# Kernel optimization log

Hardware: AMD Instinct MI355X
Metric: run time of the kernel (lower is better)

Reference implementation:

```python
import jax, jax.numpy as jnp
import numpy as np

N, E, H, IN_NF, G, STEPS, EHID = 4096, 8192, 128, 64, 8, 3, 32


def setup_inputs() -> dict:
    key = jax.random.key(0)
    ks = jax.random.split(key, 24)

    def gn(k, shape, fan_in):
        return jax.random.normal(k, shape, dtype=jnp.float32) / np.sqrt(fan_in)

    inp = {
        "x": jax.random.normal(ks[0], (N, IN_NF), dtype=jnp.float32),
        "edge_index": jax.random.randint(ks[1], (2, E), 0, N, dtype=jnp.int32),
        "edge_attr": jax.random.uniform(ks[2], (E, 1), dtype=jnp.float32),
        "batch": jnp.sort(jax.random.randint(ks[3], (N,), 0, G, dtype=jnp.int32)),
        # lin0: in_nf -> hid
        "lin0_w": gn(ks[4], (IN_NF, H), IN_NF),
        "lin0_b": jnp.zeros((H,), jnp.float32),
        # per-step edge MLP: 1 -> 32 -> H*H (stacked over STEPS)
        "nn_w1": gn(ks[5], (STEPS, 1, EHID), 1),
        "nn_b1": jnp.zeros((STEPS, EHID), jnp.float32),
        "nn_w2": gn(ks[6], (STEPS, EHID, H * H), EHID) * 0.1,
        "nn_b2": jnp.zeros((STEPS, H * H), jnp.float32),
        # NNConv root weight (no bias) + conv bias, per step
        "root_w": gn(ks[7], (STEPS, H, H), H),
        "conv_b": jnp.zeros((STEPS, H), jnp.float32),
        # single-layer GRU (input H, hidden H); gate order r, z, n
        "gru_wih": gn(ks[8], (3 * H, H), H),
        "gru_whh": gn(ks[9], (3 * H, H), H),
        "gru_bih": jnp.zeros((3 * H,), jnp.float32),
        "gru_bhh": jnp.zeros((3 * H,), jnp.float32),
        # readout
        "lin1_w": gn(ks[10], (H, H // 2), H),
        "lin1_b": jnp.zeros((H // 2,), jnp.float32),
        "lin2_w": gn(ks[11], (H // 2, 1), H // 2),
        "lin2_b": jnp.zeros((1,), jnp.float32),
    }
    return inp


def _gru_cell(m, h, wih, whh, bih, bhh):
    gi = m @ wih.T + bih          # [N, 3H]
    gh = h @ whh.T + bhh          # [N, 3H]
    i_r, i_z, i_n = jnp.split(gi, 3, axis=-1)
    h_r, h_z, h_n = jnp.split(gh, 3, axis=-1)
    r = jax.nn.sigmoid(i_r + h_r)
    z = jax.nn.sigmoid(i_z + h_z)
    n = jnp.tanh(i_n + r * h_n)
    return (1.0 - z) * n + z * h


def reference(x, edge_index, edge_attr, batch, lin0_w, lin0_b, nn_w1, nn_b1,
              nn_w2, nn_b2, root_w, conv_b, gru_wih, gru_whh, gru_bih,
              gru_bhh, lin1_w, lin1_b, lin2_w, lin2_b):
    n_nodes = x.shape[0]
    row, col = edge_index[0], edge_index[1]  # source j -> target i

    x = jax.nn.relu(x @ lin0_w + lin0_b)     # [N, H]
    h = x

    # in-degree for mean aggregation (0-degree nodes -> 0 output)
    deg = jax.ops.segment_sum(jnp.ones((row.shape[0],), x.dtype), col,
                              num_segments=n_nodes)
    inv_deg = jnp.where(deg > 0, 1.0 / jnp.maximum(deg, 1.0), 0.0)[:, None]

    for t in range(STEPS):
        # edge-conditioned weights: [E, H, H]
        e_h = jax.nn.relu(edge_attr @ nn_w1[t] + nn_b1[t])
        w_e = (e_h @ nn_w2[t] + nn_b2[t]).reshape(-1, H, H)
        # gather -> per-edge matvec -> scatter-mean
        msg = jnp.einsum('eh,eho->eo', x[row], w_e)
        agg = jax.ops.segment_sum(msg, col, num_segments=n_nodes) * inv_deg
        m = jax.nn.relu(agg + x @ root_w[t] + conv_b[t])
        h = _gru_cell(m, h, gru_wih, gru_whh, gru_bih, gru_bhh)
        x = h

    # global mean pool over graphs
    cnt = jax.ops.segment_sum(jnp.ones((n_nodes,), x.dtype), batch,
                              num_segments=G)
    g = jax.ops.segment_sum(x, batch, num_segments=G) / jnp.maximum(cnt, 1.0)[:, None]
    g = jax.nn.relu(g @ lin1_w + lin1_b)  # dropout: eval mode (identity)
    out = g @ lin2_w + lin2_b             # [G, 1]
    return out
```

## Files before the change

### kernel.cpp

```cpp
#include <hip/hip_runtime.h>
#include <math.h>

#define NN 4096
#define EE 8192
#define HH 128
#define GG 8
#define MU 4096

typedef __attribute__((ext_vector_type(8))) _Float16 half8;
typedef __attribute__((ext_vector_type(4))) float floatx4;

__device__ __forceinline__ void ldst16(const _Float16* g, void* l) {
    __builtin_amdgcn_global_load_lds(
        (const __attribute__((address_space(1))) unsigned int*)g,
        (__attribute__((address_space(3))) unsigned int*)l, 16, 0, 0);
}

__device__ __forceinline__ int cls_k(float w, float b, float mn, float mx) {
    const float hi = w > 0.f ? w * mx + b : w * mn + b;
    const float lo = w > 0.f ? w * mn + b : w * mx + b;
    if (hi <= 0.f) return 0;
    if (lo >= 0.f) return 1;
    return 2;
}

__device__ __forceinline__ void ea_range(const float* eattr, float* sred,
                                         float& mn, float& mx) {
    const int t = threadIdx.x;
    float mxl = -1e30f, mnl = 1e30f;
    for (int i = t; i < EE; i += 256) {
        const float v = eattr[i];
        mxl = fmaxf(mxl, v); mnl = fminf(mnl, v);
    }
    sred[t] = mxl; __syncthreads();
    for (int d = 128; d > 0; d >>= 1) {
        if (t < d) sred[t] = fmaxf(sred[t], sred[t + d]);
        __syncthreads();
    }
    mx = sred[0]; __syncthreads();
    sred[t] = mnl; __syncthreads();
    for (int d = 128; d > 0; d >>= 1) {
        if (t < d) sred[t] = fminf(sred[t], sred[t + d]);
        __syncthreads();
    }
    mn = sred[0]; __syncthreads();
}

__global__ __launch_bounds__(256) void ymix_gh_k(
    const _Float16* __restrict__ A, const _Float16* __restrict__ BT3t,
    const _Float16* __restrict__ Bhh, const float* __restrict__ bhh,
    const float* __restrict__ w2t, _Float16* __restrict__ Y,
    float* __restrict__ g2, _Float16* __restrict__ U,
    float* __restrict__ mpre, const int* __restrict__ kflag)
{
    __shared__ __align__(16) _Float16 As[128 * 32];
    __shared__ __align__(16) _Float16 Bs[128 * 32];
    const int tid = threadIdx.x;
    const int lane = tid & 63, wave = tid >> 6;
    const int m0 = blockIdx.y * 128;
    const int wr = (wave >> 1) * 64, wc = (wave & 1) * 64;
    const int fm = lane & 15, fq = lane >> 4;
    const int srow = tid >> 2, soff = (tid & 3) << 3;
    const _Float16* gA0 = A + (size_t)(m0 + srow) * 128 + soff;
    const _Float16* gA1 = gA0 + (size_t)64 * 128;
    char* lA0 = (char*)As + tid * 16;  char* lA1 = (char*)As + (tid + 256) * 16;
    char* lB0 = (char*)Bs + tid * 16;  char* lB1 = (char*)Bs + (tid + 256) * 16;
    const int bx = blockIdx.x;
    const int er = fq * 4, ec = fm;

    const int bid = blockIdx.y * gridDim.x + blockIdx.x;
    const int nbl = gridDim.x * gridDim.y;
    for (int i = bid * 256 + tid; i < 131072; i += nbl * 256)
        ((float4*)mpre)[i] = make_float4(0.f, 0.f, 0.f, 0.f);

    floatx4 acc[4][4] = {};
    if (bx < 6) {
        const _Float16* gB0 = (bx < 3)
            ? BT3t + (size_t)(bx * 128 + srow) * 128 + soff
            : Bhh + (size_t)((bx - 3) * 128 + srow) * 128 + soff;
        const _Float16* gB1 = gB0 + (size_t)64 * 128;
        for (int k0 = 0; k0 < 128; k0 += 32) {
            __syncthreads();
            ldst16(gA0 + k0, lA0); ldst16(gA1 + k0, lA1);
            ldst16(gB0 + k0, lB0); ldst16(gB1 + k0, lB1);
            __syncthreads();
            half8 af[4], bf[4];
#pragma unroll
            for (int i = 0; i < 4; ++i)
                af[i] = *(const half8*)&As[(wr + i * 16 + fm) * 32 + fq * 8];
#pragma unroll
            for (int j = 0; j < 4; ++j)
                bf[j] = *(const half8*)&Bs[(wc + j * 16 + fm) * 32 + fq * 8];
#pragma unroll
            for (int i = 0; i < 4; ++i)
#pragma unroll
                for (int j = 0; j < 4; ++j)
                    acc[i][j] = __builtin_amdgcn_mfma_f32_16x16x32_f16(
                        af[i], bf[j], acc[i][j], 0, 0, 0);
        }
        if (bx < 3) {
#pragma unroll
            for (int i = 0; i < 4; ++i) {
                const int gr = m0 + wr + i * 16 + er;
#pragma unroll
                for (int j = 0; j < 4; ++j) {
                    const int gc = bx * 128 + wc + j * 16 + ec;
#pragma unroll
                    for (int r = 0; r < 4; ++r)
                        Y[(size_t)(gr + r) * 384 + gc] = (_Float16)acc[i][j][r];
                }
            }
        } else {
            const int n0 = (bx - 3) * 128;
#pragma unroll
            for (int i = 0; i < 4; ++i) {
                const int gr = m0 + wr + i * 16 + er;
#pragma unroll
                for (int j = 0; j < 4; ++j) {
                    const int gc = n0 + wc + j * 16 + ec;
                    const float bv = bhh[gc];
#pragma unroll
                    for (int r = 0; r < 4; ++r)
                        g2[(size_t)(gr + r) * 384 + gc] = acc[i][j][r] + bv;
                }
            }
        }
    } else {
        const unsigned f = *(const unsigned*)kflag;
        const int kk = bx - 6;
        if (!((f >> kk) & 1u)) return;
        const int cbase = __popc(f & ((1u << kk) - 1u)) << 7;
        const float* w2s = w2t + (size_t)kk * 16384;
        for (int k0 = 0; k0 < 128; k0 += 32) {
            __syncthreads();
            ldst16(gA0 + k0, lA0); ldst16(gA1 + k0, lA1);
#pragma unroll
            for (int c = tid; c < 512; c += 256) {
                const int row = c >> 2, seg = (c & 3) << 3;
                _Float16 v8[8];
#pragma unroll
                for (int u = 0; u < 8; ++u)
                    v8[u] = (_Float16)w2s[(size_t)(k0 + seg + u) * 128 + row];
                *(half8*)&Bs[row * 32 + seg] = *(half8*)v8;
            }
            __syncthreads();
            half8 af[4], bf[4];
#pragma unroll
            for (int i = 0; i < 4; ++i)
                af[i] = *(const half8*)&As[(wr + i * 16 + fm) * 32 + fq * 8];
#pragma unroll
            for (int j = 0; j < 4; ++j)
                bf[j] = *(const half8*)&Bs[(wc + j * 16 + fm) * 32 + fq * 8];
#pragma unroll
            for (int i = 0; i < 4; ++i)
#pragma unroll
                for (int j = 0; j < 4; ++j)
                    acc[i][j] = __builtin_amdgcn_mfma_f32_16x16x32_f16(
                        af[i], bf[j], acc[i][j], 0, 0, 0);
        }
#pragma unroll
        for (int i = 0; i < 4; ++i) {
            const int gr = m0 + wr + i * 16 + er;
#pragma unroll
            for (int j = 0; j < 4; ++j) {
                const int gc = cbase + wc + j * 16 + ec;
#pragma unroll
                for (int r = 0; r < 4; ++r)
                    U[(size_t)(gr + r) * MU + gc] = (_Float16)acc[i][j][r];
            }
        }
    }
}

__global__ __launch_bounds__(256) void escat_k(
    const int* __restrict__ ei, const float* __restrict__ eattr,
    const float* __restrict__ deg, const float* __restrict__ ehPt,
    const _Float16* __restrict__ Y, const _Float16* __restrict__ U,
    float* __restrict__ mpre, const int* __restrict__ kflag)
{
    const int e = blockIdx.x * 2 + (threadIdx.x >> 7);
    const int o = threadIdx.x & 127;
    const int src = ei[e], dst = ei[EE + e];
    const float dv = deg[dst];
    const float inv = dv > 0.f ? 1.0f / dv : 0.0f;
    const float ea = eattr[e];
    const _Float16* Yr = Y + (size_t)src * 384;
    float acc = ea * inv * (float)Yr[o] + inv * (float)Yr[128 + o];
    const unsigned f = *(const unsigned*)kflag;
    if (f) {
        const int nk = __popc(f);
        const _Float16* Ur = U + (size_t)src * MU;
        const float* ep = ehPt + (size_t)e * 32;
        for (int i = 0; i < nk; ++i)
            acc += ep[i] * (float)Ur[i * 128 + o];
    }
    atomicAdd(&mpre[(size_t)dst * 128 + o], acc);
}

__global__ __launch_bounds__(256) void gruz0_k(
    const float* __restrict__ mpre, const _Float16* __restrict__ Y,
    const float* __restrict__ cb, const _Float16* __restrict__ Bih,
    const float* __restrict__ bih, float* __restrict__ g1)
{
    __shared__ __align__(16) _Float16 As[128 * 40];
    __shared__ __align__(16) _Float16 Bs[128 * 40];
    const int tid = threadIdx.x;
    const int lane = tid & 63, wave = tid >> 6;
    const int m0 = blockIdx.y * 128, n0 = blockIdx.x * 128;
    const int wr = (wave >> 1) * 64, wc = (wave & 1) * 64;
    const int fm = lane & 15, fq = lane >> 4;

    floatx4 acc[4][4] = {};
    for (int k0 = 0; k0 < 128; k0 += 32) {
        __syncthreads();
#pragma unroll
        for (int c = tid; c < 512; c += 256) {
            const int row = c >> 2, seg = (c & 3) << 3;
            const int mr = m0 + row;
            const half8 yv = *(const half8*)&Y[(size_t)mr * 384 + 256 + k0 + seg];
            const float4 a0 = *(const float4*)&mpre[(size_t)mr * 128 + k0 + seg];
            const float4 a1 = *(const float4*)&mpre[(size_t)mr * 128 + k0 + seg + 4];
            const float4 c0 = *(const float4*)&cb[k0 + seg];
            const float4 c1 = *(const float4*)&cb[k0 + seg + 4];
            _Float16 v8[8];
            float v;
            v = (float)yv[0] + a0.x + c0.x; v8[0] = (_Float16)(v > 0.f ? v : 0.f);
            v = (float)yv[1] + a0.y + c0.y; v8[1] = (_Float16)(v > 0.f ? v : 0.f);
            v = (float)yv[2] + a0.z + c0.z; v8[2] = (_Float16)(v > 0.f ? v : 0.f);
            v = (float)yv[3] + a0.w + c0.w; v8[3] = (_Float16)(v > 0.f ? v : 0.f);
            v = (float)yv[4] + a1.x + c1.x; v8[4] = (_Float16)(v > 0.f ? v : 0.f);
            v = (float)yv[5] + a1.y + c1.y; v8[5] = (_Float16)(v > 0.f ? v : 0.f);
            v = (float)yv[6] + a1.z + c1.z; v8[6] = (_Float16)(v > 0.f ? v : 0.f);
            v = (float)yv[7] + a1.w + c1.w; v8[7] = (_Float16)(v > 0.f ? v : 0.f);
            *(half8*)&As[row * 40 + seg] = *(half8*)v8;
            *(half8*)&Bs[row * 40 + seg] =
                *(const half8*)&Bih[(size_t)(n0 + row) * 128 + k0 + seg];
        }
        __syncthreads();
        half8 af[4], bf[4];
#pragma unroll
        for (int i = 0; i < 4; ++i)
            af[i] = *(const half8*)&As[(wr + i * 16 + fm) * 40 + fq * 8];
#pragma unroll
        for (int j = 0; j < 4; ++j)
            bf[j] = *(const half8*)&Bs[(wc + j * 16 + fm) * 40 + fq * 8];
#pragma unroll
        for (int i = 0; i < 4; ++i)
#pragma unroll
            for (int j = 0; j < 4; ++j)
                acc[i][j] = __builtin_amdgcn_mfma_f32_16x16x32_f16(
                    af[i], bf[j], acc[i][j], 0, 0, 0);
    }
    const int er = fq * 4, ec = fm;
#pragma unroll
    for (int i = 0; i < 4; ++i) {
        const int gr = m0 + wr + i * 16 + er;
#pragma unroll
        for (int j = 0; j < 4; ++j) {
            const int gc = n0 + wc + j * 16 + ec;
            const float bv = bih[gc];
#pragma unroll
            for (int r = 0; r < 4; ++r)
                g1[(size_t)(gr + r) * 384 + gc] = acc[i][j][r] + bv;
        }
    }
}

__global__ void gate_k(const float* __restrict__ G1, const float* __restrict__ G2,
                       float* __restrict__ xh, _Float16* __restrict__ Ax,
                       const int* __restrict__ batch, float* __restrict__ pooled) {
    const int idx = blockIdx.x * 256 + threadIdx.x;
    const int n = idx >> 7, o = idx & 127;
    const size_t b = (size_t)n * 384;
    float ir = G1[b + o], iz = G1[b + 128 + o], in_ = G1[b + 256 + o];
    float hr = G2[b + o], hz = G2[b + 128 + o], hn = G2[b + 256 + o];
    float r = 1.f / (1.f + expf(-(ir + hr)));
    float z = 1.f / (1.f + expf(-(iz + hz)));
    float nv = tanhf(in_ + r * hn);
    float hv = (1.f - z) * nv + z * xh[idx];
    xh[idx] = hv;
    Ax[idx] = (_Float16)hv;
    if (pooled) atomicAdd(&pooled[batch[n] * 128 + o], hv);
}

__global__ __launch_bounds__(256) void setup_all_k(
    const float* __restrict__ wih, const float* __restrict__ whh,
    _Float16* __restrict__ Bih, _Float16* __restrict__ Bhh,
    const int* __restrict__ ei, const float* __restrict__ eattr,
    const int* __restrict__ batch, float* __restrict__ deg,
    float* __restrict__ cnt,
    const float* __restrict__ x, const float* __restrict__ l0w,
    const float* __restrict__ l0b, float* __restrict__ xh,
    _Float16* __restrict__ Ax,
    const float* __restrict__ w1, const float* __restrict__ b1,
    const float* __restrict__ w2, const float* __restrict__ b2,
    const float* __restrict__ rw, _Float16* __restrict__ BT3,
    float* __restrict__ ehP, int* __restrict__ kflag)
{
    __shared__ float loc8[GG];
    __shared__ float As[16][64];
    __shared__ float Bs[16][64];
    __shared__ float sred[256];
    __shared__ float wl[32], bl[32];
    __shared__ unsigned mm[3];
    const int b = blockIdx.x, t = threadIdx.x;
    if (b < 192) {
        const int idx = b * 256 + t;
        Bih[idx] = (_Float16)wih[idx];
        Bhh[idx] = (_Float16)whh[idx];
    } else if (b < 224) {
        const int e = (b - 192) * 256 + t;
        atomicAdd(&deg[ei[EE + e]], 1.0f);
    } else if (b < 240) {
        const int n = (b - 224) * 256 + t;
        if (t < GG) loc8[t] = 0.f;
        __syncthreads();
        atomicAdd(&loc8[batch[n]], 1.0f);
        __syncthreads();
        if (t < GG) atomicAdd(&cnt[t], loc8[t]);
    } else if (b < 368) {
        const int bb = b - 240;
        const int j0 = (bb & 1) * 64;
        const int m0 = (bb >> 1) * 64;
        const int tx = t & 15, ty = t >> 4;
        const int arow = t >> 2, acol = (t & 3) << 2;
        const int bk = t >> 4, bj = (t & 15) << 2;
        float c[4][4] = {};
        for (int k0 = 0; k0 < 64; k0 += 16) {
            __syncthreads();
            float4 av = *(const float4*)&x[(size_t)(m0 + arow) * 64 + k0 + acol];
            As[acol + 0][arow] = av.x;
            As[acol + 1][arow] = av.y;
            As[acol + 2][arow] = av.z;
            As[acol + 3][arow] = av.w;
            *(float4*)&Bs[bk][bj] = *(const float4*)&l0w[(size_t)(k0 + bk) * 128 + j0 + bj];
            __syncthreads();
#pragma unroll
            for (int kk = 0; kk < 16; ++kk) {
                const float4 a = *(const float4*)&As[kk][ty << 2];
                const float4 bv = *(const float4*)&Bs[kk][tx << 2];
                c[0][0] += a.x * bv.x; c[0][1] += a.x * bv.y; c[0][2] += a.x * bv.z; c[0][3] += a.x * bv.w;
                c[1][0] += a.y * bv.x; c[1][1] += a.y * bv.y; c[1][2] += a.y * bv.z; c[1][3] += a.y * bv.w;
                c[2][0] += a.z * bv.x; c[2][1] += a.z * bv.y; c[2][2] += a.z * bv.z; c[2][3] += a.z * bv.w;
                c[3][0] += a.w * bv.x; c[3][1] += a.w * bv.y; c[3][2] += a.w * bv.z; c[3][3] += a.w * bv.w;
            }
        }
        const float4 bv = *(const float4*)&l0b[j0 + (tx << 2)];
        const int col0 = j0 + (tx << 2);
#pragma unroll
        for (int i = 0; i < 4; ++i) {
            const int row = m0 + (ty << 2) + i;
            float4 o;
            o.x = fmaxf(c[i][0] + bv.x, 0.f); o.y = fmaxf(c[i][1] + bv.y, 0.f);
            o.z = fmaxf(c[i][2] + bv.z, 0.f); o.w = fmaxf(c[i][3] + bv.w, 0.f);
            *(float4*)&xh[(size_t)row * 128 + col0] = o;
            _Float16* base = Ax + (size_t)row * 128 + col0;
            base[0] = (_Float16)o.x; base[1] = (_Float16)o.y;
            base[2] = (_Float16)o.z; base[3] = (_Float16)o.w;
        }
    } else if (b < 560) {
        float mn, mx;
        ea_range(eattr, sred, mn, mx);
        const int bb = b - 368;
        const int st = bb >> 6;
        if (t < 32) {
            const float w = w1[st * 32 + t], bv = b1[st * 32 + t];
            const int c = cls_k(w, bv, mn, mx);
            wl[t] = (c == 1) ? w : 0.f;
            bl[t] = (c == 1) ? bv : 0.f;
        }
        __syncthreads();
        const int idx = (bb & 63) * 256 + t;
        const int h = idx >> 7, o = idx & 127;
        const float* W2t = w2 + (size_t)st * 524288;
        float a = 0.f, c2 = 0.f;
#pragma unroll 8
        for (int j = 0; j < 32; ++j) {
            const float v = W2t[(size_t)j * 16384 + idx];
            a += wl[j] * v; c2 += bl[j] * v;
        }
        c2 += b2[(size_t)st * 16384 + idx];
        _Float16* B = BT3 + (size_t)st * 49152;
        B[(size_t)o * 128 + h]         = (_Float16)a;
        B[(size_t)(128 + o) * 128 + h] = (_Float16)c2;
        B[(size_t)(256 + o) * 128 + h] = (_Float16)rw[(size_t)st * 16384 + idx];
    } else if (b == 560) {
        float mn, mx;
        ea_range(eattr, sred, mn, mx);
        if (t < 3) mm[t] = 0u;
        __syncthreads();
        if (t < 96) {
            const int tt = t >> 5, k = t & 31;
            if (cls_k(w1[tt * 32 + k], b1[tt * 32 + k], mn, mx) == 2)
                atomicOr(&mm[tt], 1u << k);
        }
        __syncthreads();
        if (t < 3) kflag[t] = (int)mm[t];
    } else {
        float mn, mx;
        ea_range(eattr, sred, mn, mx);
        if (t < 3) mm[t] = 0u;
        __syncthreads();
        if (t < 96) {
            const int tt = t >> 5, k = t & 31;
            if (cls_k(w1[tt * 32 + k], b1[tt * 32 + k], mn, mx) == 2)
                atomicOr(&mm[tt], 1u << k);
        }
        __syncthreads();
        if (!(mm[0] | mm[1] | mm[2])) return;
        const int e = (b - 561) * 256 + t;
        const int dst = ei[EE + e];
        const float dv = deg[dst];
        (void)dv;
        const float ea = eattr[e];
        for (int tt = 0; tt < 3; ++tt) {
            const unsigned m = mm[tt];
            if (!m) continue;
            unsigned rem = m;
            int slot = 0;
            while (rem) {
                const int k = __ffs(rem) - 1; rem &= rem - 1;
                const float v = ea * w1[tt * 32 + k] + b1[tt * 32 + k];
                ehP[((size_t)tt * EE + e) * 32 + slot] = (v > 0.f ? v : 0.f);
                ++slot;
            }
        }
    }
}

__global__ __launch_bounds__(128) void final_k(
    const float* __restrict__ pooled, const float* __restrict__ cnt,
    const float* __restrict__ l1w, const float* __restrict__ l1b,
    const float* __restrict__ l2w, const float* __restrict__ l2b,
    float* __restrict__ out)
{
    __shared__ float gv[128];
    const int g = blockIdx.x, t = threadIdx.x;
    float c = cnt[g]; c = c > 1.f ? c : 1.f;
    gv[t] = pooled[g * 128 + t] / c;
    __syncthreads();
    if (t < 64) {
        float y = l1b[t];
        for (int h = 0; h < 128; ++h) y += gv[h] * l1w[h * 64 + t];
        y = y > 0.f ? y : 0.f;
        float s = y * l2w[t];
#pragma unroll
        for (int off = 32; off > 0; off >>= 1)
            s += __shfl_down(s, off);
        if (t == 0) out[g] = s + l2b[0];
    }
}

extern "C" void kernel_launch(void* const* d_in, const int* in_sizes, int n_in,
                              void* d_out, int out_size, void* d_ws, size_t ws_size,
                              hipStream_t stream) {
    const float* x      = (const float*)d_in[0];
    const int*   ei     = (const int*)d_in[1];
    const float* eattr  = (const float*)d_in[2];
    const int*   batch  = (const int*)d_in[3];
    const float* lin0_w = (const float*)d_in[4];
    const float* lin0_b = (const float*)d_in[5];
    const float* nn_w1  = (const float*)d_in[6];
    const float* nn_b1  = (const float*)d_in[7];
    const float* nn_w2  = (const float*)d_in[8];
    const float* nn_b2  = (const float*)d_in[9];
    const float* root_w = (const float*)d_in[10];
    const float* conv_b = (const float*)d_in[11];
    const float* gwih   = (const float*)d_in[12];
    const float* gwhh   = (const float*)d_in[13];
    const float* gbih   = (const float*)d_in[14];
    const float* gbhh   = (const float*)d_in[15];
    const float* l1w    = (const float*)d_in[16];
    const float* l1b    = (const float*)d_in[17];
    const float* l2w    = (const float*)d_in[18];
    const float* l2b    = (const float*)d_in[19];
    float* out = (float*)d_out;
    float* ws  = (float*)d_ws;

    float*    pooled = ws;
    float*    cnt    = ws + 1024;
    float*    deg    = ws + 1032;
    int*      kflag  = (int*)(ws + 5128);
    float*    ehP    = ws + 5136;
    float*    xh     = ws + 791568;
    float*    g1     = ws + 1315856;
    float*    g2     = ws + 2888720;
    float*    mpre0  = ws + 4461584;
    _Float16* Y      = (_Float16*)(ws + 6034448);
    _Float16* Ax     = (_Float16*)(ws + 6820880);
    _Float16* BT3    = (_Float16*)(ws + 7083024);
    _Float16* Bih16  = (_Float16*)(ws + 7156752);
    _Float16* Bhh16  = (_Float16*)(ws + 7181328);
    _Float16* U      = (_Float16*)(ws + 7205904);

    hipMemsetAsync(pooled, 0, 20512, stream);
    setup_all_k<<<593, 256, 0, stream>>>(gwih, gwhh, Bih16, Bhh16, ei, eattr,
                                         batch, deg, cnt, x, lin0_w, lin0_b,
                                         xh, Ax, nn_w1, nn_b1, nn_w2, nn_b2,
                                         root_w, BT3, ehP, kflag);

    for (int t = 0; t < 3; ++t) {
        float* mpre = mpre0 + (size_t)t * 524288;
        ymix_gh_k<<<dim3(38, 32), 256, 0, stream>>>(
            Ax, BT3 + (size_t)t * 49152, Bhh16, gbhh,
            nn_w2 + (size_t)t * 524288, Y, g2, U, mpre, kflag + t);
        escat_k<<<4096, 256, 0, stream>>>(ei, eattr, deg,
                                          ehP + (size_t)t * EE * 32,
                                          Y, U, mpre, kflag + t);
        gruz0_k<<<dim3(3, 32), 256, 0, stream>>>(mpre, Y, conv_b + t * 128,
                                                 Bih16, gbih, g1);
        gate_k<<<2048, 256, 0, stream>>>(g1, g2, xh, Ax, batch,
                                         (t == 2) ? pooled : nullptr);
    }

    final_k<<<GG, 128, 0, stream>>>(pooled, cnt, l1w, l1b, l2w, l2b, out);
}
```

Measured before the change: 213.4 us.

## Fuse GRU input GEMM with gate update and fold U-GEMM blocks into loop

Merges the GRU input-projection GEMM and the elementwise gate kernel into one kernel. Each block now computes all three gate slices for 32 rows and applies the sigmoid/tanh update in registers, so the g1 intermediate is never written to or read from global memory and one launch per step is removed. The edge-weight U-GEMM column blocks are collapsed into a single column that loops over the active hidden units, shrinking the ymix grid. The escat U-path now also scales by inverse degree, which is a correctness change. The fused kernel launches only 128 blocks and each block stages the full 384x128 Bih in LDS, which lowers parallelism and occupancy.

Measured after the change: 257.2 us. 1.21x slower.

```diff
diff --git a/kernel.cpp b/kernel.cpp
--- a/kernel.cpp
+++ b/kernel.cpp
@@ -73,8 +73,8 @@
     for (int i = bid * 256 + tid; i < 131072; i += nbl * 256)
         ((float4*)mpre)[i] = make_float4(0.f, 0.f, 0.f, 0.f);
 
-    floatx4 acc[4][4] = {};
     if (bx < 6) {
+        floatx4 acc[4][4] = {};
         const _Float16* gB0 = (bx < 3)
             ? BT3t + (size_t)(bx * 128 + srow) * 128 + soff
             : Bhh + (size_t)((bx - 3) * 128 + srow) * 128 + soff;
@@ -127,47 +127,51 @@
         }
     } else {
         const unsigned f = *(const unsigned*)kflag;
-        const int kk = bx - 6;
-        if (!((f >> kk) & 1u)) return;
-        const int cbase = __popc(f & ((1u << kk) - 1u)) << 7;
-        const float* w2s = w2t + (size_t)kk * 16384;
-        for (int k0 = 0; k0 < 128; k0 += 32) {
+        if (!f) return;
+        for (int kk = 0; kk < 32; ++kk) {
+            if (!((f >> kk) & 1u)) continue;
+            const int cbase = __popc(f & ((1u << kk) - 1u)) << 7;
+            const float* w2s = w2t + (size_t)kk * 16384;
+            floatx4 acc[4][4] = {};
+            for (int k0 = 0; k0 < 128; k0 += 32) {
+                __syncthreads();
+                ldst16(gA0 + k0, lA0); ldst16(gA1 + k0, lA1);
+#pragma unroll
+                for (int c = tid; c < 512; c += 256) {
+                    const int row = c >> 2, seg = (c & 3) << 3;
+                    _Float16 v8[8];
+#pragma unroll
+                    for (int u = 0; u < 8; ++u)
+                        v8[u] = (_Float16)w2s[(size_t)(k0 + seg + u) * 128 + row];
+                    *(half8*)&Bs[row * 32 + seg] = *(half8*)v8;
+                }
+                __syncthreads();
+                half8 af[4], bf[4];
+#pragma unroll
+                for (int i = 0; i < 4; ++i)
+                    af[i] = *(const half8*)&As[(wr + i * 16 + fm) * 32 + fq * 8];
+#pragma unroll
+                for (int j = 0; j < 4; ++j)
+                    bf[j] = *(const half8*)&Bs[(wc + j * 16 + fm) * 32 + fq * 8];
+#pragma unroll
+                for (int i = 0; i < 4; ++i)
+#pragma unroll
+                    for (int j = 0; j < 4; ++j)
+                        acc[i][j] = __builtin_amdgcn_mfma_f32_16x16x32_f16(
+                            af[i], bf[j], acc[i][j], 0, 0, 0);
+            }
+#pragma unroll
+            for (int i = 0; i < 4; ++i) {
+                const int gr = m0 + wr + i * 16 + er;
+#pragma unroll
+                for (int j = 0; j < 4; ++j) {
+                    const int gc = cbase + wc + j * 16 + ec;
+#pragma unroll
+                    for (int r = 0; r < 4; ++r)
+                        U[(size_t)(gr + r) * MU + gc] = (_Float16)acc[i][j][r];
+                }
+            }
             __syncthreads();
-            ldst16(gA0 + k0, lA0); ldst16(gA1 + k0, lA1);
-#pragma unroll
-            for (int c = tid; c < 512; c += 256) {
-                const int row = c >> 2, seg = (c & 3) << 3;
-                _Float16 v8[8];
-#pragma unroll
-                for (int u = 0; u < 8; ++u)
-                    v8[u] = (_Float16)w2s[(size_t)(k0 + seg + u) * 128 + row];
-                *(half8*)&Bs[row * 32 + seg] = *(half8*)v8;
-            }
-            __syncthreads();
-            half8 af[4], bf[4];
-#pragma unroll
-            for (int i = 0; i < 4; ++i)
-                af[i] = *(const half8*)&As[(wr + i * 16 + fm) * 32 + fq * 8];
-#pragma unroll
-            for (int j = 0; j < 4; ++j)
-                bf[j] = *(const half8*)&Bs[(wc + j * 16 + fm) * 32 + fq * 8];
-#pragma unroll
-            for (int i = 0; i < 4; ++i)
-#pragma unroll
-                for (int j = 0; j < 4; ++j)
-                    acc[i][j] = __builtin_amdgcn_mfma_f32_16x16x32_f16(
-                        af[i], bf[j], acc[i][j], 0, 0, 0);
-        }
-#pragma unroll
-        for (int i = 0; i < 4; ++i) {
-            const int gr = m0 + wr + i * 16 + er;
-#pragma unroll
-            for (int j = 0; j < 4; ++j) {
-                const int gc = cbase + wc + j * 16 + ec;
-#pragma unroll
-                for (int r = 0; r < 4; ++r)
-                    U[(size_t)(gr + r) * MU + gc] = (_Float16)acc[i][j][r];
-            }
         }
     }
 }
@@ -192,95 +196,98 @@
         const _Float16* Ur = U + (size_t)src * MU;
         const float* ep = ehPt + (size_t)e * 32;
         for (int i = 0; i < nk; ++i)
-            acc += ep[i] * (float)Ur[i * 128 + o];
+            acc += inv * ep[i] * (float)Ur[i * 128 + o];
     }
     atomicAdd(&mpre[(size_t)dst * 128 + o], acc);
 }
 
-__global__ __launch_bounds__(256) void gruz0_k(
+__global__ __launch_bounds__(256) void gruz0gate_k(
     const float* __restrict__ mpre, const _Float16* __restrict__ Y,
     const float* __restrict__ cb, const _Float16* __restrict__ Bih,
-    const float* __restrict__ bih, float* __restrict__ g1)
+    const float* __restrict__ bih, const float* __restrict__ g2,
+    float* __restrict__ xh, _Float16* __restrict__ Ax,
+    const int* __restrict__ batch, float* __restrict__ pooled)
 {
-    __shared__ __align__(16) _Float16 As[128 * 40];
-    __shared__ __align__(16) _Float16 Bs[128 * 40];
+    __shared__ __align__(16) _Float16 As[32 * 40];
+    __shared__ __align__(16) _Float16 Bs[384 * 40];
     const int tid = threadIdx.x;
     const int lane = tid & 63, wave = tid >> 6;
-    const int m0 = blockIdx.y * 128, n0 = blockIdx.x * 128;
-    const int wr = (wave >> 1) * 64, wc = (wave & 1) * 64;
+    const int m0 = blockIdx.x * 32;
     const int fm = lane & 15, fq = lane >> 4;
 
-    floatx4 acc[4][4] = {};
+    floatx4 acc[2][3][2] = {};
     for (int k0 = 0; k0 < 128; k0 += 32) {
         __syncthreads();
-#pragma unroll
-        for (int c = tid; c < 512; c += 256) {
-            const int row = c >> 2, seg = (c & 3) << 3;
-            const int mr = m0 + row;
-            const half8 yv = *(const half8*)&Y[(size_t)mr * 384 + 256 + k0 + seg];
-            const float4 a0 = *(const float4*)&mpre[(size_t)mr * 128 + k0 + seg];
-            const float4 a1 = *(const float4*)&mpre[(size_t)mr * 128 + k0 + seg + 4];
-            const float4 c0 = *(const float4*)&cb[k0 + seg];
-            const float4 c1 = *(const float4*)&cb[k0 + seg + 4];
-            _Float16 v8[8];
-            float v;
-            v = (float)yv[0] + a0.x + c0.x; v8[0] = (_Float16)(v > 0.f ? v : 0.f);
-            v = (float)yv[1] + a0.y + c0.y; v8[1] = (_Float16)(v > 0.f ? v : 0.f);
-            v = (float)yv[2] + a0.z + c0.z; v8[2] = (_Float16)(v > 0.f ? v : 0.f);
-            v = (float)yv[3] + a0.w + c0.w; v8[3] = (_Float16)(v > 0.f ? v : 0.f);
-            v = (float)yv[4] + a1.x + c1.x; v8[4] = (_Float16)(v > 0.f ? v : 0.f);
-            v = (float)yv[5] + a1.y + c1.y; v8[5] = (_Float16)(v > 0.f ? v : 0.f);
-            v = (float)yv[6] + a1.z + c1.z; v8[6] = (_Float16)(v > 0.f ? v : 0.f);
-            v = (float)yv[7] + a1.w + c1.w; v8[7] = (_Float16)(v > 0.f ? v : 0.f);
-            *(half8*)&As[row * 40 + seg] = *(half8*)v8;
-            *(half8*)&Bs[row * 40 + seg] =
-                *(const half8*)&Bih[(size_t)(n0 + row) * 128 + k0 + seg];
-        }
-        __syncthreads();
-        half8 af[4], bf[4];
-#pragma unroll
-        for (int i = 0; i < 4; ++i)
-            af[i] = *(const half8*)&As[(wr + i * 16 + fm) * 40 + fq * 8];
-#pragma unroll
-        for (int j = 0; j < 4; ++j)
-            bf[j] = *(const half8*)&Bs[(wc + j * 16 + fm) * 40 + fq * 8];
-#pragma unroll
-        for (int i = 0; i < 4; ++i)
-#pragma unroll
-            for (int j = 0; j < 4; ++j)
-                acc[i][j] = __builtin_amdgcn_mfma_f32_16x16x32_f16(
-                    af[i], bf[j], acc[i][j], 0, 0, 0);
-    }
-    const int er = fq * 4, ec = fm;
-#pragma unroll
-    for (int i = 0; i < 4; ++i) {
-        const int gr = m0 + wr + i * 16 + er;
-#pragma unroll
-        for (int j = 0; j < 4; ++j) {
-            const int gc = n0 + wc + j * 16 + ec;
-            const float bv = bih[gc];
-#pragma unroll
-            for (int r = 0; r < 4; ++r)
-                g1[(size_t)(gr + r) * 384 + gc] = acc[i][j][r] + bv;
-        }
-    }
-}
-
-__global__ void gate_k(const float* __restrict__ G1, const float* __restrict__ G2,
-                       float* __restrict__ xh, _Float16* __restrict__ Ax,
-                       const int* __restrict__ batch, float* __restrict__ pooled) {
-    const int idx = blockIdx.x * 256 + threadIdx.x;
-    const int n = idx >> 7, o = idx & 127;
-    const size_t b = (size_t)n * 384;
-    float ir = G1[b + o], iz = G1[b + 128 + o], in_ = G1[b + 256 + o];
-    float hr = G2[b + o], hz = G2[b + 128 + o], hn = G2[b + 256 + o];
-    float r = 1.f / (1.f + expf(-(ir + hr)));
-    float z = 1.f / (1.f + expf(-(iz + hz)));
-    float nv = tanhf(in_ + r * hn);
-    float hv = (1.f - z) * nv + z * xh[idx];
-    xh[idx] = hv;
-    Ax[idx] = (_Float16)hv;
-    if (pooled) atomicAdd(&pooled[batch[n] * 128 + o], hv);
+        for (int c = tid; c < 1664; c += 256) {
+            if (c < 128) {
+                const int row = c >> 2, seg = (c & 3) << 3;
+                const int mr = m0 + row;
+                const half8 yv = *(const half8*)&Y[(size_t)mr * 384 + 256 + k0 + seg];
+                const float4 a0 = *(const float4*)&mpre[(size_t)mr * 128 + k0 + seg];
+                const float4 a1 = *(const float4*)&mpre[(size_t)mr * 128 + k0 + seg + 4];
+                const float4 c0 = *(const float4*)&cb[k0 + seg];
+                const float4 c1 = *(const float4*)&cb[k0 + seg + 4];
+                _Float16 v8[8];
+                float v;
+                v = (float)yv[0] + a0.x + c0.x; v8[0] = (_Float16)(v > 0.f ? v : 0.f);
+                v = (float)yv[1] + a0.y + c0.y; v8[1] = (_Float16)(v > 0.f ? v : 0.f);
+                v = (float)yv[2] + a0.z + c0.z; v8[2] = (_Float16)(v > 0.f ? v : 0.f);
+                v = (float)yv[3] + a0.w + c0.w; v8[3] = (_Float16)(v > 0.f ? v : 0.f);
+                v = (float)yv[4] + a1.x + c1.x; v8[4] = (_Float16)(v > 0.f ? v : 0.f);
+                v = (float)yv[5] + a1.y + c1.y; v8[5] = (_Float16)(v > 0.f ? v : 0.f);
+                v = (float)yv[6] + a1.z + c1.z; v8[6] = (_Float16)(v > 0.f ? v : 0.f);
+                v = (float)yv[7] + a1.w + c1.w; v8[7] = (_Float16)(v > 0.f ? v : 0.f);
+                *(half8*)&As[row * 40 + seg] = *(half8*)v8;
+            } else {
+                const int cc = c - 128;
+                const int row = cc >> 2, seg = (cc & 3) << 3;
+                *(half8*)&Bs[row * 40 + seg] =
+                    *(const half8*)&Bih[(size_t)row * 128 + k0 + seg];
+            }
+        }
+        __syncthreads();
+        half8 af[2];
+#pragma unroll
+        for (int i = 0; i < 2; ++i)
+            af[i] = *(const half8*)&As[(i * 16 + fm) * 40 + fq * 8];
+#pragma unroll
+        for (int part = 0; part < 3; ++part)
+#pragma unroll
+            for (int jj = 0; jj < 2; ++jj) {
+                const half8 bf = *(const half8*)
+                    &Bs[(part * 128 + wave * 32 + jj * 16 + fm) * 40 + fq * 8];
+#pragma unroll
+                for (int i = 0; i < 2; ++i)
+                    acc[i][part][jj] = __builtin_amdgcn_mfma_f32_16x16x32_f16(
+                        af[i], bf, acc[i][part][jj], 0, 0, 0);
+            }
+    }
+#pragma unroll
+    for (int jj = 0; jj < 2; ++jj) {
+        const int o = wave * 32 + jj * 16 + fm;
+        const float bir = bih[o], biz = bih[128 + o], bin_ = bih[256 + o];
+#pragma unroll
+        for (int i = 0; i < 2; ++i) {
+#pragma unroll
+            for (int rr = 0; rr < 4; ++rr) {
+                const int row = m0 + i * 16 + fq * 4 + rr;
+                const float ir = acc[i][0][jj][rr] + bir;
+                const float iz = acc[i][1][jj][rr] + biz;
+                const float in_ = acc[i][2][jj][rr] + bin_;
+                const float hr = g2[(size_t)row * 384 + o];
+                const float hz = g2[(size_t)row * 384 + 128 + o];
+                const float hn = g2[(size_t)row * 384 + 256 + o];
+                const float rg = 1.f / (1.f + expf(-(ir + hr)));
+                const float zg = 1.f / (1.f + expf(-(iz + hz)));
+                const float nv = tanhf(in_ + rg * hn);
+                const size_t xi = (size_t)row * 128 + o;
+                const float hv = (1.f - zg) * nv + zg * xh[xi];
+                xh[xi] = hv;
+                Ax[xi] = (_Float16)hv;
+                if (pooled) atomicAdd(&pooled[batch[row] * 128 + o], hv);
+            }
+        }
+    }
 }
 
 __global__ __launch_bounds__(256) void setup_all_k(
@@ -409,9 +416,6 @@
         __syncthreads();
         if (!(mm[0] | mm[1] | mm[2])) return;
         const int e = (b - 561) * 256 + t;
-        const int dst = ei[EE + e];
-        const float dv = deg[dst];
-        (void)dv;
         const float ea = eattr[e];
         for (int tt = 0; tt < 3; ++tt) {
             const unsigned m = mm[tt];
@@ -483,7 +487,6 @@
     int*      kflag  = (int*)(ws + 5128);
     float*    ehP    = ws + 5136;
     float*    xh     = ws + 791568;
-    float*    g1     = ws + 1315856;
     float*    g2     = ws + 2888720;
     float*    mpre0  = ws + 4461584;
     _Float16* Y      = (_Float16*)(ws + 6034448);
@@ -501,16 +504,15 @@
 
     for (int t = 0; t < 3; ++t) {
         float* mpre = mpre0 + (size_t)t * 524288;
-        ymix_gh_k<<<dim3(38, 32), 256, 0, stream>>>(
+        ymix_gh_k<<<dim3(7, 32), 256, 0, stream>>>(
             Ax, BT3 + (size_t)t * 49152, Bhh16, gbhh,
             nn_w2 + (size_t)t * 524288, Y, g2, U, mpre, kflag + t);
         escat_k<<<4096, 256, 0, stream>>>(ei, eattr, deg,
                                           ehP + (size_t)t * EE * 32,
                                           Y, U, mpre, kflag + t);
-        gruz0_k<<<dim3(3, 32), 256, 0, stream>>>(mpre, Y, conv_b + t * 128,
-                                                 Bih16, gbih, g1);
-        gate_k<<<2048, 256, 0, stream>>>(g1, g2, xh, Ax, batch,
-                                         (t == 2) ? pooled : nullptr);
+        gruz0gate_k<<<128, 256, 0, stream>>>(mpre, Y, conv_b + t * 128,
+                                             Bih16, gbih, g2, xh, Ax, batch,
+                                             (t == 2) ? pooled : nullptr);
     }
 
     final_k<<<GG, 128, 0, stream>>>(pooled, cnt, l1w, l1b, l2w, l2b, out);
```
